# Optimization experiments

Measured on AMD Instinct MI355X. Metric: run time of the kernel, lower is better.

## Reference

```python
import jax, jax.numpy as jnp
import numpy as np

B, L_IN, D_MODEL, CONV_D, KSIZE = 16, 512, 384, 1536, 3
MEL_MAX = 4096
LN_EPS = 1e-5


def _conv1d_same(h, w, b):
    # h: [B, C_in, L], w: [C_out, C_in, K] -> [B, C_out, L]
    y = jax.lax.conv_general_dilated(h, w, window_strides=(1,), padding='SAME',
                                     dimension_numbers=('NCH', 'OIH', 'NCH'))
    return y + b[None, :, None]


def _layernorm(x, g, b):
    m = jnp.mean(x, -1, keepdims=True)
    v = jnp.mean((x - m) ** 2, -1, keepdims=True)
    return (x - m) * jax.lax.rsqrt(v + LN_EPS) * g + b


def _ffn(x, wa, ba, wb, bb):
    # Conv1D_FFT: conv(d_model->conv_d) ReLU conv(conv_d->d_model) ReLU
    h = jnp.transpose(x, (0, 2, 1))
    h = jax.nn.relu(_conv1d_same(h, wa, ba))
    h = jax.nn.relu(_conv1d_same(h, wb, bb))
    return jnp.transpose(h, (0, 2, 1))


def _dur_pred(x, w1, b1, w2, b2, g1, be1, w3, b3, w4, b4, g2, be2, wl, bl):
    h = _ffn(x, w1, b1, w2, b2)
    h = _layernorm(h, g1, be1)  # dropout is identity at eval
    h = _ffn(h, w3, b3, w4, b4)
    h = _layernorm(h, g2, be2)
    return (h @ wl + bl)[..., 0]  # [B, L_in], squeeze(-1)


def _length_regulate(x, dur, mel_max_len):
    # Equivalent to alignment @ x where alignment[b,t,j]=1 iff cum[b,j-1] <= t < cum[b,j],
    # padded with zeros out to mel_max_len (original pads output to mel_max_len).
    cum = jnp.cumsum(dur, axis=-1)                        # [B, L_in]
    total = cum[:, -1]                                    # [B]
    t = jnp.arange(mel_max_len, dtype=cum.dtype)          # [T]
    idx = jax.vmap(lambda c: jnp.searchsorted(c, t, side='right'))(cum)  # [B, T]
    idx = jnp.minimum(idx, x.shape[1] - 1)
    out = jnp.take_along_axis(x, idx[:, :, None], axis=1)  # [B, T, D]
    mask = (t[None, :] < total[:, None])[..., None]
    return out * mask


def setup_inputs() -> dict:
    key = jax.random.key(0)
    ks = jax.random.split(key, 8)
    def nrm(k, shape):
        return jax.random.normal(k, shape, jnp.float32) * 0.02
    return {
        'x': jax.random.normal(ks[0], (B, L_IN, D_MODEL), jnp.float32),
        'target': jax.random.randint(ks[1], (B, L_IN), 0, 8, jnp.int32),
        'mel_max_len': MEL_MAX,
        'w1': nrm(ks[2], (CONV_D, D_MODEL, KSIZE)), 'b1': jnp.zeros((CONV_D,), jnp.float32),
        'w2': nrm(ks[3], (D_MODEL, CONV_D, KSIZE)), 'b2': jnp.zeros((D_MODEL,), jnp.float32),
        'g1': jnp.ones((D_MODEL,), jnp.float32), 'be1': jnp.zeros((D_MODEL,), jnp.float32),
        'w3': nrm(ks[4], (CONV_D, D_MODEL, KSIZE)), 'b3': jnp.zeros((CONV_D,), jnp.float32),
        'w4': nrm(ks[5], (D_MODEL, CONV_D, KSIZE)), 'b4': jnp.zeros((D_MODEL,), jnp.float32),
        'g2': jnp.ones((D_MODEL,), jnp.float32), 'be2': jnp.zeros((D_MODEL,), jnp.float32),
        'wl': nrm(ks[6], (D_MODEL, 1)), 'bl': jnp.zeros((1,), jnp.float32),
    }


def reference(x, target, mel_max_len, w1, b1, w2, b2, g1, be1, w3, b3, w4, b4, g2, be2, wl, bl):
    dur_preds = _dur_pred(x, w1, b1, w2, b2, g1, be1, w3, b3, w4, b4, g2, be2, wl, bl)
    output = _length_regulate(x, target, mel_max_len)
    return (output, dur_preds)
```

## Files before the change

### kernel.cpp

```cpp
#include <hip/hip_runtime.h>
#include <hip/hip_bf16.h>
#include <cstddef>
#include <cstdint>

#define NB 16
#define LIN 512
#define DM 384
#define DC 1536
#define MELMAX 4096
#define LN_EPS 1e-5f

typedef __bf16 bf16x8 __attribute__((ext_vector_type(8)));
typedef float f32x4 __attribute__((ext_vector_type(4)));

#define GL2LDS(gp, lp)                                                                \
    __builtin_amdgcn_global_load_lds((const __attribute__((address_space(1))) void*)(gp), \
                                     (__attribute__((address_space(3))) void*)(lp), 16, 0, 0)

__device__ __forceinline__ float wred(float v) {
#pragma unroll
    for (int m = 32; m >= 1; m >>= 1) v += __shfl_xor(v, m, 64);
    return v;
}

__device__ __forceinline__ unsigned short f2bf(float f) {
    __hip_bfloat16 h = __float2bfloat16(f);
    return *reinterpret_cast<unsigned short*>(&h);
}

__device__ __forceinline__ float bf2f(unsigned short u) {
    return __uint_as_float(((unsigned)u) << 16);
}


__global__ void cumsum_kernel(const int* __restrict__ tgt, int* __restrict__ cum) {
    __shared__ int s[LIN];
    const int b = blockIdx.x, tid = threadIdx.x;
    s[tid] = tgt[b * LIN + tid];
    __syncthreads();
    for (int off = 1; off < LIN; off <<= 1) {
        int v = (tid >= off) ? s[tid - off] : 0;
        __syncthreads();
        s[tid] += v;
        __syncthreads();
    }
    cum[b * LIN + tid] = s[tid];
}


__global__ __launch_bounds__(256) void gather_kernel(const float* __restrict__ x,
                                                     const int* __restrict__ cum,
                                                     float* __restrict__ out) {
    const int wid = (blockIdx.x * 256 + threadIdx.x) >> 6;
    const int lane = threadIdx.x & 63;
    const int b = wid >> 12;
    const int t = wid & (MELMAX - 1);
    const int* c = cum + b * LIN;
    const int total = c[LIN - 1];
    float4* orow = reinterpret_cast<float4*>(out + ((size_t)b * MELMAX + t) * DM);
    if (t < total) {
        int lo = 0, hi = LIN;
        while (lo < hi) { int mid = (lo + hi) >> 1; if (c[mid] > t) hi = mid; else lo = mid + 1; }
        const int idx = lo < (LIN - 1) ? lo : (LIN - 1);
        const float4* xrow = reinterpret_cast<const float4*>(x + ((size_t)b * LIN + idx) * DM);
#pragma unroll
        for (int j = 0; j < 2; ++j) {
            const int p = lane + 64 * j;
            if (p < DM / 4) orow[p] = xrow[p];
        }
    } else {
        const float4 z = make_float4(0.f, 0.f, 0.f, 0.f);
#pragma unroll
        for (int j = 0; j < 2; ++j) {
            const int p = lane + 64 * j;
            if (p < DM / 4) orow[p] = z;
        }
    }
}


#define ZPAD_BLKS 96
#define CASTX_BLKS 3072
#define WCAST_BLKS 2304

__global__ void prep_kernel(const float* __restrict__ x, unsigned short* __restrict__ xb,
                            unsigned short* __restrict__ hbig, unsigned short* __restrict__ h2b,
                            const float* __restrict__ w1, const float* __restrict__ w2,
                            const float* __restrict__ w3, const float* __restrict__ w4,
                            unsigned short* __restrict__ o1, unsigned short* __restrict__ o2,
                            unsigned short* __restrict__ o3, unsigned short* __restrict__ o4) {
    const int bid = blockIdx.x, tid = threadIdx.x;
    if (bid < ZPAD_BLKS) {
        const int buf = bid >> 5, rem = bid & 31;
        const int b = rem >> 1, row = (rem & 1) ? (LIN + 1) : 0;
        unsigned short* p = buf == 0 ? xb : (buf == 1 ? hbig : h2b);
        const int rl = buf == 1 ? DC : DM;
        unsigned short* base = p + ((size_t)b * (LIN + 2) + row) * rl;
        for (int c = tid; c < rl; c += 256) base[c] = 0;
        return;
    }
    if (bid < ZPAD_BLKS + CASTX_BLKS) {
        const int idx = (bid - ZPAD_BLKS) * 256 + tid;
        const float4 v = reinterpret_cast<const float4*>(x)[idx];
        const int e = idx * 4;
        const int b = e / (LIN * DM);
        const int rem = e - b * (LIN * DM);
        const int l = rem / DM;
        const int c = rem - l * DM;
        ushort4 o;
        o.x = f2bf(v.x); o.y = f2bf(v.y); o.z = f2bf(v.z); o.w = f2bf(v.w);
        *reinterpret_cast<ushort4*>(xb + ((size_t)b * (LIN + 2) + l + 1) * DM + c) = o;
        return;
    }
    const int j = bid - ZPAD_BLKS - CASTX_BLKS;
    const int which = j / WCAST_BLKS;
    const int idx = (j - which * WCAST_BLKS) * 256 + tid;
    const float* w = which == 0 ? w1 : which == 1 ? w2 : which == 2 ? w3 : w4;
    unsigned short* gg = which == 0 ? o1 : which == 1 ? o2 : which == 2 ? o3 : o4;
    const int CI = (which == 0 || which == 2) ? DM : DC;
    const int co = idx / CI, ci = idx - co * CI;
    const float* p = w + (size_t)idx * 3;
    unsigned short* o = gg + (size_t)co * (3 * CI) + ci;
    o[0 * CI] = f2bf(p[0]);
    o[1 * CI] = f2bf(p[1]);
    o[2 * CI] = f2bf(p[2]);
}


template <int CI, int CO>
__global__ __launch_bounds__(256, 3) void conv_mfma_kernel(const unsigned short* __restrict__ in,
                                                           const unsigned short* __restrict__ wg,
                                                           const float* __restrict__ bias,
                                                           unsigned short* __restrict__ out) {
    constexpr int BM = 128, BN = 64, BK = 32;
    constexpr int KC = CI / BK;
    constexpr int AGRP = 9;
    constexpr int GPT = BN / 16;
    constexpr int BGRP = 3 * GPT;
    constexpr int NW_N = BN / 32;
    constexpr int NT = CO / BN;
    constexpr int NCONV = NB * (LIN / BM) * NT;

    __shared__ __align__(16) unsigned short As[2][AGRP * 512];
    __shared__ __align__(16) unsigned short Bs[2][BGRP * 512];

    const int tid = threadIdx.x;
    const int lane = tid & 63;
    const int wv = tid >> 6;

    const int orig = blockIdx.x;
    const int q = NCONV >> 3, xcd = orig & 7, o = orig >> 3;
    const int wgid = xcd * q + o;

    const int mg = wgid / NT;
    const int nt = wgid - mg * NT;
    const int b = mg >> 2;
    const int l0 = (mg & 3) * BM;
    const int n0 = nt * BN;

    const int wr = wv >> 1, wc = wv & 1;

    const unsigned short* inb = in + (size_t)b * (LIN + 2) * CI;

    f32x4 acc[4][NW_N];
#pragma unroll
    for (int m = 0; m < 4; ++m)
#pragma unroll
        for (int n = 0; n < NW_N; ++n) acc[m][n] = (f32x4){0.f, 0.f, 0.f, 0.f};

    const int lrow = lane >> 2;
    const int lch = lane & 3;
    const int fr = lane & 15, kg = lane >> 4;

    const unsigned short* aroot = inb + (size_t)l0 * CI;
    const unsigned short* broot = wg + (size_t)n0 * (3 * CI);

    const int aswz = (lch ^ (lrow & 3)) * 8;
    const int bfr = lane & 15, bkg = lane >> 4;

#define STAGE(c, kb)                                                                      \
    do {                                                                                  \
        const unsigned short* abase = aroot + (kb) * BK;                                  \
        _Pragma("unroll")                                                                 \
        for (int g = wv; g < AGRP; g += 4)                                                \
            GL2LDS(abase + (size_t)(g * 16 + lrow) * CI + aswz, &As[c][g * 512]);         \
        const unsigned short* bbase = broot + (kb) * BK;                                  \
        _Pragma("unroll")                                                                 \
        for (int g2 = wv; g2 < BGRP; g2 += 4) {                                           \
            const int t = g2 / GPT, gr = g2 - t * GPT;                                    \
            GL2LDS(bbase + (size_t)(gr * 16 + bfr) * (3 * CI) + (size_t)t * CI + bkg * 8, \
                   &Bs[c][g2 * 512]);                                                     \
        }                                                                                 \
    } while (0)

#define COMPUTE(c)                                                                        \
    do {                                                                                  \
        _Pragma("unroll")                                                                 \
        for (int t = 0; t < 3; ++t) {                                                     \
            bf16x8 aF[4], bF[NW_N];                                                       \
            _Pragma("unroll")                                                             \
            for (int m = 0; m < 4; ++m) {                                                 \
                const int r = t + wr * 64 + m * 16 + fr;                                  \
                aF[m] = *reinterpret_cast<const bf16x8*>(                                 \
                    &As[c][r * BK + ((kg ^ (r & 3)) * 8)]);                               \
            }                                                                             \
            _Pragma("unroll")                                                             \
            for (int n = 0; n < NW_N; ++n)                                                \
                bF[n] = *reinterpret_cast<const bf16x8*>(                                 \
                    &Bs[c][(t * GPT + wc * NW_N + n) * 512 + kg * 128 + fr * 8]);         \
            __builtin_amdgcn_s_setprio(1);                                                \
            _Pragma("unroll")                                                             \
            for (int m = 0; m < 4; ++m)                                                   \
                _Pragma("unroll")                                                         \
                for (int n = 0; n < NW_N; ++n)                                            \
                    acc[m][n] =                                                           \
                        __builtin_amdgcn_mfma_f32_16x16x32_bf16(aF[m], bF[n], acc[m][n],  \
                                                                0, 0, 0);                 \
            __builtin_amdgcn_s_setprio(0);                                                \
        }                                                                                 \
    } while (0)

    STAGE(0, 0);
    STAGE(1, 1);
#pragma unroll 1
    for (int kb = 0; kb < KC; ++kb) {
        const int cur = kb & 1;
        if (wv == 0)
            asm volatile("s_waitcnt vmcnt(6)" ::: "memory");
        else
            asm volatile("s_waitcnt vmcnt(5)" ::: "memory");
        __builtin_amdgcn_sched_barrier(0);
        __builtin_amdgcn_s_barrier();
        __builtin_amdgcn_sched_barrier(0);
        COMPUTE(cur);
        asm volatile("s_waitcnt lgkmcnt(0)" ::: "memory");
        __builtin_amdgcn_sched_barrier(0);
        __builtin_amdgcn_s_barrier();
        __builtin_amdgcn_sched_barrier(0);
        int nk = kb + 2;
        if (nk >= KC) nk -= KC;
        STAGE(cur, nk);
    }
#undef STAGE
#undef COMPUTE

    const int fq = lane >> 4;
    float bv[NW_N];
#pragma unroll
    for (int n = 0; n < NW_N; ++n) bv[n] = bias[n0 + wc * (BN / 2) + n * 16 + fr];
    unsigned short* outb = out + (size_t)b * (LIN + 2) * CO;
#pragma unroll
    for (int m = 0; m < 4; ++m)
#pragma unroll
        for (int qy = 0; qy < 4; ++qy) {
            const int grow = l0 + wr * 64 + m * 16 + fq * 4 + qy + 1;
            unsigned short* orow = outb + (size_t)grow * CO + n0 + wc * (BN / 2) + fr;
#pragma unroll
            for (int n = 0; n < NW_N; ++n) {
                const float v = fmaxf(acc[m][n][qy] + bv[n], 0.f);
                orow[n * 16] = f2bf(v);
            }
        }
}


__global__ void ln_kernel(unsigned short* __restrict__ h, const float* __restrict__ g,
                          const float* __restrict__ be) {
    const int row = blockIdx.x, lane = threadIdx.x;
    const int b = row >> 9, l = row & (LIN - 1);
    unsigned short* hr = h + ((size_t)b * (LIN + 2) + l + 1) * DM;
    float v[6];
    float s = 0.f;
#pragma unroll
    for (int j = 0; j < 6; ++j) { v[j] = bf2f(hr[lane + 64 * j]); s += v[j]; }
    s = wred(s);
    const float mean = s * (1.f / DM);
    float vs = 0.f;
#pragma unroll
    for (int j = 0; j < 6; ++j) { const float d = v[j] - mean; vs += d * d; }
    vs = wred(vs);
    const float rstd = rsqrtf(vs * (1.f / DM) + LN_EPS);
#pragma unroll
    for (int j = 0; j < 6; ++j) {
        const int c = lane + 64 * j;
        hr[c] = f2bf((v[j] - mean) * rstd * g[c] + be[c]);
    }
}


__global__ void ln_linear_kernel(const unsigned short* __restrict__ h, const float* __restrict__ g,
                                 const float* __restrict__ be, const float* __restrict__ wl,
                                 const float* __restrict__ bl, float* __restrict__ dur) {
    const int row = blockIdx.x, lane = threadIdx.x;
    const int b = row >> 9, l = row & (LIN - 1);
    const unsigned short* hr = h + ((size_t)b * (LIN + 2) + l + 1) * DM;
    float v[6];
    float s = 0.f;
#pragma unroll
    for (int j = 0; j < 6; ++j) { v[j] = bf2f(hr[lane + 64 * j]); s += v[j]; }
    s = wred(s);
    const float mean = s * (1.f / DM);
    float vs = 0.f;
#pragma unroll
    for (int j = 0; j < 6; ++j) { const float d = v[j] - mean; vs += d * d; }
    vs = wred(vs);
    const float rstd = rsqrtf(vs * (1.f / DM) + LN_EPS);
    float dot = 0.f;
#pragma unroll
    for (int j = 0; j < 6; ++j) {
        const int c = lane + 64 * j;
        dot += ((v[j] - mean) * rstd * g[c] + be[c]) * wl[c];
    }
    dot = wred(dot);
    if (lane == 0) dur[row] = dot + bl[0];
}


extern "C" void kernel_launch(void* const* d_in, const int* in_sizes, int n_in,
                              void* d_out, int out_size, void* d_ws, size_t ws_size,
                              hipStream_t stream) {
    const float* x   = (const float*)d_in[0];
    const int*   tgt = (const int*)d_in[1];
    const float* w1  = (const float*)d_in[3];
    const float* b1  = (const float*)d_in[4];
    const float* w2  = (const float*)d_in[5];
    const float* b2  = (const float*)d_in[6];
    const float* g1  = (const float*)d_in[7];
    const float* be1 = (const float*)d_in[8];
    const float* w3  = (const float*)d_in[9];
    const float* b3  = (const float*)d_in[10];
    const float* w4  = (const float*)d_in[11];
    const float* b4  = (const float*)d_in[12];
    const float* g2  = (const float*)d_in[13];
    const float* be2 = (const float*)d_in[14];
    const float* wl  = (const float*)d_in[15];
    const float* bl  = (const float*)d_in[16];

    float* out = (float*)d_out;
    float* dur = out + (size_t)NB * MELMAX * DM;

    unsigned short* ws = (unsigned short*)d_ws;
    unsigned short* xb   = ws;
    unsigned short* hbig = xb + (size_t)NB * (LIN + 2) * DM;
    unsigned short* h2b  = hbig + (size_t)NB * (LIN + 2) * DC;
    unsigned short* wg1  = h2b + (size_t)NB * (LIN + 2) * DM;
    unsigned short* wg2  = wg1 + (size_t)DC * 3 * DM;
    unsigned short* wg3  = wg2 + (size_t)DM * 3 * DC;
    unsigned short* wg4  = wg3 + (size_t)DC * 3 * DM;
    int* cum = (int*)(wg4 + (size_t)DM * 3 * DC);

    cumsum_kernel<<<NB, LIN, 0, stream>>>(tgt, cum);
    gather_kernel<<<(NB * MELMAX) / 4, 256, 0, stream>>>(x, cum, out);

    prep_kernel<<<ZPAD_BLKS + CASTX_BLKS + 4 * WCAST_BLKS, 256, 0, stream>>>(
        x, xb, hbig, h2b, w1, w2, w3, w4, wg1, wg2, wg3, wg4);

    conv_mfma_kernel<DM, DC><<<NB * (LIN / 128) * (DC / 64), 256, 0, stream>>>(xb, wg1, b1, hbig);
    conv_mfma_kernel<DC, DM><<<NB * (LIN / 128) * (DM / 64), 256, 0, stream>>>(hbig, wg2, b2, h2b);
    ln_kernel<<<NB * LIN, 64, 0, stream>>>(h2b, g1, be1);
    conv_mfma_kernel<DM, DC><<<NB * (LIN / 128) * (DC / 64), 256, 0, stream>>>(h2b, wg3, b3, hbig);
    conv_mfma_kernel<DC, DM><<<NB * (LIN / 128) * (DM / 64), 256, 0, stream>>>(hbig, wg4, b4, xb);
    ln_linear_kernel<<<NB * LIN, 64, 0, stream>>>(xb, g2, be2, wl, bl, dur);
}
```

Before: 235.5 us.

## Process two N-tiles per workgroup in the expanding conv via a chained K loop

The conv kernel gains an NTIL parameter. With NTIL=2 it runs two consecutive 64-wide output-channel tiles in one workgroup, chaining their K loops into a single pipelined loop with a second accumulator set. For the DM->DC convs this halves the grid and amortizes prologue and epilogue cost. The pipeline stays full across the tile boundary instead of draining. The A tile is still reloaded per tile, so the main saving is launch and fill overhead. The extra accumulators raise register pressure, which could hurt occupancy under launch_bounds(256,3).

Measured after the change: 232.5 us. Within noise of the previous version (-1.3%).

```diff
diff --git a/kernel.cpp b/kernel.cpp
--- a/kernel.cpp
+++ b/kernel.cpp
@@ -127,7 +127,7 @@
 }
 
 
-template <int CI, int CO>
+template <int CI, int CO, int NTIL>
 __global__ __launch_bounds__(256, 3) void conv_mfma_kernel(const unsigned short* __restrict__ in,
                                                            const unsigned short* __restrict__ wg,
                                                            const float* __restrict__ bias,
@@ -138,8 +138,9 @@
     constexpr int GPT = BN / 16;
     constexpr int BGRP = 3 * GPT;
     constexpr int NW_N = BN / 32;
-    constexpr int NT = CO / BN;
-    constexpr int NCONV = NB * (LIN / BM) * NT;
+    constexpr int NPJ = CO / BN / NTIL;
+    constexpr int NCONV = NB * (LIN / BM) * NPJ;
+    constexpr int TOTK = NTIL * KC;
 
     __shared__ __align__(16) unsigned short As[2][AGRP * 512];
     __shared__ __align__(16) unsigned short Bs[2][BGRP * 512];
@@ -152,39 +153,43 @@
     const int q = NCONV >> 3, xcd = orig & 7, o = orig >> 3;
     const int wgid = xcd * q + o;
 
-    const int mg = wgid / NT;
-    const int nt = wgid - mg * NT;
+    const int mg = wgid / NPJ;
+    const int j = wgid - mg * NPJ;
     const int b = mg >> 2;
     const int l0 = (mg & 3) * BM;
-    const int n0 = nt * BN;
+    const int n0 = j * (BN * NTIL);
 
     const int wr = wv >> 1, wc = wv & 1;
 
     const unsigned short* inb = in + (size_t)b * (LIN + 2) * CI;
 
-    f32x4 acc[4][NW_N];
+    f32x4 acc[4][NW_N], acc2[4][NW_N];
 #pragma unroll
     for (int m = 0; m < 4; ++m)
 #pragma unroll
-        for (int n = 0; n < NW_N; ++n) acc[m][n] = (f32x4){0.f, 0.f, 0.f, 0.f};
+        for (int n = 0; n < NW_N; ++n) {
+            acc[m][n] = (f32x4){0.f, 0.f, 0.f, 0.f};
+            acc2[m][n] = (f32x4){0.f, 0.f, 0.f, 0.f};
+        }
 
     const int lrow = lane >> 2;
     const int lch = lane & 3;
     const int fr = lane & 15, kg = lane >> 4;
 
     const unsigned short* aroot = inb + (size_t)l0 * CI;
-    const unsigned short* broot = wg + (size_t)n0 * (3 * CI);
+    const unsigned short* broot0 = wg + (size_t)n0 * (3 * CI);
+    const unsigned short* broot1 = broot0 + (size_t)BN * (3 * CI);
 
     const int aswz = (lch ^ (lrow & 3)) * 8;
     const int bfr = lane & 15, bkg = lane >> 4;
 
-#define STAGE(c, kb)                                                                      \
+#define STAGE(c, kb, BR)                                                                  \
     do {                                                                                  \
         const unsigned short* abase = aroot + (kb) * BK;                                  \
         _Pragma("unroll")                                                                 \
         for (int g = wv; g < AGRP; g += 4)                                                \
             GL2LDS(abase + (size_t)(g * 16 + lrow) * CI + aswz, &As[c][g * 512]);         \
-        const unsigned short* bbase = broot + (kb) * BK;                                  \
+        const unsigned short* bbase = (BR) + (kb) * BK;                                   \
         _Pragma("unroll")                                                                 \
         for (int g2 = wv; g2 < BGRP; g2 += 4) {                                           \
             const int t = g2 / GPT, gr = g2 - t * GPT;                                    \
@@ -193,7 +198,7 @@
         }                                                                                 \
     } while (0)
 
-#define COMPUTE(c)                                                                        \
+#define COMPUTE(c, ACC)                                                                   \
     do {                                                                                  \
         _Pragma("unroll")                                                                 \
         for (int t = 0; t < 3; ++t) {                                                     \
@@ -213,17 +218,17 @@
             for (int m = 0; m < 4; ++m)                                                   \
                 _Pragma("unroll")                                                         \
                 for (int n = 0; n < NW_N; ++n)                                            \
-                    acc[m][n] =                                                           \
-                        __builtin_amdgcn_mfma_f32_16x16x32_bf16(aF[m], bF[n], acc[m][n],  \
+                    ACC[m][n] =                                                           \
+                        __builtin_amdgcn_mfma_f32_16x16x32_bf16(aF[m], bF[n], ACC[m][n],  \
                                                                 0, 0, 0);                 \
             __builtin_amdgcn_s_setprio(0);                                                \
         }                                                                                 \
     } while (0)
 
-    STAGE(0, 0);
-    STAGE(1, 1);
+    STAGE(0, 0, broot0);
+    STAGE(1, 1, broot0);
 #pragma unroll 1
-    for (int kb = 0; kb < KC; ++kb) {
+    for (int kb = 0; kb < TOTK; ++kb) {
         const int cur = kb & 1;
         if (wv == 0)
             asm volatile("s_waitcnt vmcnt(6)" ::: "memory");
@@ -232,35 +237,49 @@
         __builtin_amdgcn_sched_barrier(0);
         __builtin_amdgcn_s_barrier();
         __builtin_amdgcn_sched_barrier(0);
-        COMPUTE(cur);
+        if (NTIL == 1 || kb < KC)
+            COMPUTE(cur, acc);
+        else
+            COMPUTE(cur, acc2);
         asm volatile("s_waitcnt lgkmcnt(0)" ::: "memory");
         __builtin_amdgcn_sched_barrier(0);
         __builtin_amdgcn_s_barrier();
         __builtin_amdgcn_sched_barrier(0);
         int nk = kb + 2;
-        if (nk >= KC) nk -= KC;
-        STAGE(cur, nk);
+        if (nk >= TOTK) nk -= TOTK;
+        const unsigned short* br = broot0;
+        int ak = nk;
+        if (NTIL == 2 && nk >= KC) { br = broot1; ak = nk - KC; }
+        STAGE(cur, ak, br);
     }
 #undef STAGE
 #undef COMPUTE
 
     const int fq = lane >> 4;
-    float bv[NW_N];
-#pragma unroll
-    for (int n = 0; n < NW_N; ++n) bv[n] = bias[n0 + wc * (BN / 2) + n * 16 + fr];
     unsigned short* outb = out + (size_t)b * (LIN + 2) * CO;
-#pragma unroll
-    for (int m = 0; m < 4; ++m)
-#pragma unroll
-        for (int qy = 0; qy < 4; ++qy) {
-            const int grow = l0 + wr * 64 + m * 16 + fq * 4 + qy + 1;
-            unsigned short* orow = outb + (size_t)grow * CO + n0 + wc * (BN / 2) + fr;
-#pragma unroll
-            for (int n = 0; n < NW_N; ++n) {
-                const float v = fmaxf(acc[m][n][qy] + bv[n], 0.f);
-                orow[n * 16] = f2bf(v);
-            }
-        }
+#define EPI(ACC, NBASE)                                                                   \
+    do {                                                                                  \
+        float bv[NW_N];                                                                   \
+        _Pragma("unroll")                                                                 \
+        for (int n = 0; n < NW_N; ++n) bv[n] = bias[(NBASE) + wc * (BN / 2) + n * 16 + fr]; \
+        _Pragma("unroll")                                                                 \
+        for (int m = 0; m < 4; ++m)                                                       \
+            _Pragma("unroll")                                                             \
+            for (int qy = 0; qy < 4; ++qy) {                                              \
+                const int grow = l0 + wr * 64 + m * 16 + fq * 4 + qy + 1;                 \
+                unsigned short* orow =                                                    \
+                    outb + (size_t)grow * CO + (NBASE) + wc * (BN / 2) + fr;              \
+                _Pragma("unroll")                                                         \
+                for (int n = 0; n < NW_N; ++n) {                                          \
+                    const float v = fmaxf(ACC[m][n][qy] + bv[n], 0.f);                    \
+                    orow[n * 16] = f2bf(v);                                               \
+                }                                                                         \
+            }                                                                             \
+    } while (0)
+
+    EPI(acc, n0);
+    if (NTIL == 2) EPI(acc2, n0 + BN);
+#undef EPI
 }
 
 
@@ -355,10 +374,10 @@
     prep_kernel<<<ZPAD_BLKS + CASTX_BLKS + 4 * WCAST_BLKS, 256, 0, stream>>>(
         x, xb, hbig, h2b, w1, w2, w3, w4, wg1, wg2, wg3, wg4);
 
-    conv_mfma_kernel<DM, DC><<<NB * (LIN / 128) * (DC / 64), 256, 0, stream>>>(xb, wg1, b1, hbig);
-    conv_mfma_kernel<DC, DM><<<NB * (LIN / 128) * (DM / 64), 256, 0, stream>>>(hbig, wg2, b2, h2b);
+    conv_mfma_kernel<DM, DC, 2><<<NB * (LIN / 128) * (DC / 128), 256, 0, stream>>>(xb, wg1, b1, hbig);
+    conv_mfma_kernel<DC, DM, 1><<<NB * (LIN / 128) * (DM / 64), 256, 0, stream>>>(hbig, wg2, b2, h2b);
     ln_kernel<<<NB * LIN, 64, 0, stream>>>(h2b, g1, be1);
-    conv_mfma_kernel<DM, DC><<<NB * (LIN / 128) * (DC / 64), 256, 0, stream>>>(h2b, wg3, b3, hbig);
-    conv_mfma_kernel<DC, DM><<<NB * (LIN / 128) * (DM / 64), 256, 0, stream>>>(hbig, wg4, b4, xb);
+    conv_mfma_kernel<DM, DC, 2><<<NB * (LIN / 128) * (DC / 128), 256, 0, stream>>>(h2b, wg3, b3, hbig);
+    conv_mfma_kernel<DC, DM, 1><<<NB * (LIN / 128) * (DM / 64), 256, 0, stream>>>(hbig, wg4, b4, xb);
     ln_linear_kernel<<<NB * LIN, 64, 0, stream>>>(xb, g2, be2, wl, bl, dur);
 }
```
